# Kernel optimization log

Measured on AMD Instinct MI355X. Metric: run time of the kernel, lower is better.

## Reference

```python
import jax, jax.numpy as jnp
import numpy as np
import math

N_EMBD = 1024
N_HEAD = 16
HEAD_DIM = N_EMBD // N_HEAD
SCALE = 1.0 / math.sqrt(HEAD_DIM)


def setup_inputs() -> dict:
    key = jax.random.key(0)
    ks = jax.random.split(key, 5)
    B, S = 1, 4096
    std = 0.02
    x = jax.random.normal(ks[0], (B, S, N_EMBD), dtype=jnp.float32)
    # Linear weights stored as [in, out] (transposed vs torch storage; same math)
    w_qkv = jax.random.normal(ks[1], (N_EMBD, 3 * N_EMBD), dtype=jnp.float32) * std
    b_qkv = jnp.zeros((3 * N_EMBD,), dtype=jnp.float32)
    w_out = jax.random.normal(ks[2], (N_EMBD, N_EMBD), dtype=jnp.float32) * std
    b_out = jnp.zeros((N_EMBD,), dtype=jnp.float32)
    return {"x": x, "w_qkv": w_qkv, "b_qkv": b_qkv, "w_out": w_out, "b_out": b_out}


def reference(x, w_qkv, b_qkv, w_out, b_out):
    B, S, D = x.shape
    qkv = x @ w_qkv + b_qkv                      # [B, S, 3D]
    q, k, v = jnp.split(qkv, 3, axis=-1)
    # [B, H, S, d]
    q = q.reshape(B, S, N_HEAD, HEAD_DIM).transpose(0, 2, 1, 3)
    k = k.reshape(B, S, N_HEAD, HEAD_DIM).transpose(0, 2, 1, 3)
    v = v.reshape(B, S, N_HEAD, HEAD_DIM).transpose(0, 2, 1, 3)
    scores = jnp.einsum("bhqd,bhkd->bhqk", q, k) * SCALE  # [B, H, S, S]
    causal = jnp.tril(jnp.ones((S, S), dtype=bool))
    scores = jnp.where(causal, scores, -jnp.inf)
    attn = jax.nn.softmax(scores, axis=-1)
    out = jnp.einsum("bhqk,bhkd->bhqd", attn, v)  # [B, H, S, d]
    out = out.transpose(0, 2, 1, 3).reshape(B, S, D)
    return out @ w_out + b_out
```

## Files before the change

kernel.cpp:

```cpp
#include <hip/hip_runtime.h>
#include <hip/hip_bf16.h>
#include <cstdint>

typedef __bf16 bf16x8 __attribute__((ext_vector_type(8)));
typedef float  f32x4  __attribute__((ext_vector_type(4)));

#define S_LEN 4096
#define D_EMB 1024
#define N3    3072
#define HDIM  64

__device__ __forceinline__ unsigned short f2bf(float f) {
    union { unsigned int i; float f; } v; v.f = f;
    unsigned int i = v.i;
    return (unsigned short)((i + 0x7FFFu + ((i >> 16) & 1u)) >> 16);
}

__device__ __forceinline__ void async16(const void* g, void* l) {
    __builtin_amdgcn_global_load_lds(
        (const __attribute__((address_space(1))) unsigned int*)g,
        (__attribute__((address_space(3))) unsigned int*)l,
        16, 0, 0);
}

__global__ void convert_f32_bf16(const float* __restrict__ src,
                                 unsigned short* __restrict__ dst, int n8) {
    const int i = blockIdx.x * blockDim.x + threadIdx.x;
    if (i >= n8) return;
    float4 f0 = *(const float4*)&src[i * 8];
    float4 f1 = *(const float4*)&src[i * 8 + 4];
    union { uint4 q; unsigned short s[8]; } o;
    o.s[0]=f2bf(f0.x); o.s[1]=f2bf(f0.y); o.s[2]=f2bf(f0.z); o.s[3]=f2bf(f0.w);
    o.s[4]=f2bf(f1.x); o.s[5]=f2bf(f1.y); o.s[6]=f2bf(f1.z); o.s[7]=f2bf(f1.w);
    *(uint4*)&dst[i * 8] = o.q;
}

__global__ void transpose_f32_to_bf16(const float* __restrict__ src,
                                      unsigned short* __restrict__ dst,
                                      int R, int ld, int c0) {
    __shared__ float tile[32][33];
    const int tx = threadIdx.x, ty = threadIdx.y;
    const int r0 = blockIdx.y * 32, cc0 = blockIdx.x * 32;
    for (int i = 0; i < 32; i += 8)
        tile[ty + i][tx] = src[(size_t)(r0 + ty + i) * ld + c0 + cc0 + tx];
    __syncthreads();
    for (int i = 0; i < 32; i += 8)
        dst[(size_t)(cc0 + ty + i) * R + r0 + tx] = f2bf(tile[tx][ty + i]);
}

__global__ void transpose_bf16(const unsigned short* __restrict__ src,
                               unsigned short* __restrict__ dst,
                               int R, int ld, int c0) {
    __shared__ unsigned short tile[32][33];
    const int tx = threadIdx.x, ty = threadIdx.y;
    const int r0 = blockIdx.y * 32, cc0 = blockIdx.x * 32;
    for (int i = 0; i < 32; i += 8)
        tile[ty + i][tx] = src[(size_t)(r0 + ty + i) * ld + c0 + cc0 + tx];
    __syncthreads();
    for (int i = 0; i < 32; i += 8)
        dst[(size_t)(cc0 + ty + i) * R + r0 + tx] = tile[tx][ty + i];
}

template <bool OUT_F32>
__global__ __launch_bounds__(256) void gemm_bt_bias(
    const unsigned short* __restrict__ A,
    const unsigned short* __restrict__ BT,
    const float* __restrict__ bias,
    void* __restrict__ Cp,
    int M, int N, int K)
{
    __shared__ __align__(16) unsigned short As[128 * 32];
    __shared__ __align__(16) unsigned short Bs[128 * 32];
    const int tid  = threadIdx.x;
    const int wave = tid >> 6, lane = tid & 63;
    const int q4 = lane >> 4, l16 = lane & 15;
    const int m0 = blockIdx.y * 128, n0 = blockIdx.x * 128;
    const int wm = (wave >> 1) * 64, wn = (wave & 1) * 64;

    f32x4 acc[4][4] = {};

    const int srow = wave * 32 + (lane >> 2);
    const int scol = (lane & 3) * 8;

    for (int k0 = 0; k0 < K; k0 += 32) {
        __syncthreads();
        for (int i = 0; i < 2; ++i) {
            const int r = srow + i * 16;
            async16(A  + (size_t)(m0 + r) * K + k0 + scol,
                    &As[(wave * 32 + i * 16) * 32 + lane * 8]);
            async16(BT + (size_t)(n0 + r) * K + k0 + scol,
                    &Bs[(wave * 32 + i * 16) * 32 + lane * 8]);
        }
        __syncthreads();

        bf16x8 af[4], bfr[4];
        for (int mi = 0; mi < 4; ++mi)
            af[mi] = *(const bf16x8*)&As[(wm + mi * 16 + l16) * 32 + q4 * 8];
        for (int ni = 0; ni < 4; ++ni)
            bfr[ni] = *(const bf16x8*)&Bs[(wn + ni * 16 + l16) * 32 + q4 * 8];
        for (int mi = 0; mi < 4; ++mi)
            for (int ni = 0; ni < 4; ++ni)
                acc[mi][ni] = __builtin_amdgcn_mfma_f32_16x16x32_bf16(
                    af[mi], bfr[ni], acc[mi][ni], 0, 0, 0);
    }

    for (int ni = 0; ni < 4; ++ni) {
        const int col = n0 + wn + ni * 16 + l16;
        const float bv = bias[col];
        for (int mi = 0; mi < 4; ++mi) {
            const int row = m0 + wm + mi * 16 + q4 * 4;
            for (int r = 0; r < 4; ++r) {
                const float val = acc[mi][ni][r] + bv;
                if constexpr (OUT_F32)
                    ((float*)Cp)[(size_t)(row + r) * N + col] = val;
                else
                    ((unsigned short*)Cp)[(size_t)(row + r) * N + col] = f2bf(val);
            }
        }
    }
}

#define LDP 72
__global__ __launch_bounds__(256) void attn_flash(
    const unsigned short* __restrict__ qkv,
    const unsigned short* __restrict__ Vt,
    unsigned short* __restrict__ X2)
{
    __shared__ __align__(16) unsigned short Ks[64 * LDP];
    __shared__ __align__(16) unsigned short Vs[64 * LDP];
    __shared__ __align__(16) unsigned short Ps[4 * 16 * LDP];
    const int tid  = threadIdx.x;
    const int wave = tid >> 6, lane = tid & 63;
    const int q4 = lane >> 4, l16 = lane & 15;
    const int h  = blockIdx.y;

    const int x = blockIdx.x, hg = blockIdx.y >> 2;
    int qt;
    if      (hg == 0) qt = x;
    else if (hg == 1) qt = 63 - x;
    else if (hg == 2) qt = (x + 16) & 63;
    else              qt = (47 - x) & 63;
    const int q0 = qt * 64;

    bf16x8 aq[2];
    {
        const unsigned short* qp =
            qkv + (size_t)(q0 + wave * 16 + l16) * N3 + h * HDIM + q4 * 8;
        aq[0] = *(const bf16x8*)(qp);
        aq[1] = *(const bf16x8*)(qp + 32);
    }

    float l_part[4] = {0.f, 0.f, 0.f, 0.f};
    f32x4 o[4] = {};

    const int rr = tid >> 3;
    const int cc = (tid & 7) * 8;
    const int ntile = qt + 1;

    for (int t = 0; t < ntile; ++t) {
        const int kv0 = t * 64;
        uint4 kv_a = *(const uint4*)&qkv[(size_t)(kv0 + rr)      * N3 + D_EMB + h * HDIM + cc];
        uint4 kv_b = *(const uint4*)&qkv[(size_t)(kv0 + 32 + rr) * N3 + D_EMB + h * HDIM + cc];
        uint4 vt_a = *(const uint4*)&Vt [(size_t)(h * HDIM + rr)      * S_LEN + kv0 + cc];
        uint4 vt_b = *(const uint4*)&Vt [(size_t)(h * HDIM + 32 + rr) * S_LEN + kv0 + cc];
        __syncthreads();
        *(uint4*)&Ks[rr * LDP + cc]        = kv_a;
        *(uint4*)&Ks[(32 + rr) * LDP + cc] = kv_b;
        *(uint4*)&Vs[rr * LDP + cc]        = vt_a;
        *(uint4*)&Vs[(32 + rr) * LDP + cc] = vt_b;
        __syncthreads();

        f32x4 sacc[4] = {};
        for (int kk = 0; kk < 2; ++kk)
            for (int nt = 0; nt < 4; ++nt) {
                bf16x8 b = *(const bf16x8*)&Ks[(nt * 16 + l16) * LDP + kk * 32 + q4 * 8];
                sacc[nt] = __builtin_amdgcn_mfma_f32_16x16x32_bf16(
                    aq[kk], b, sacc[nt], 0, 0, 0);
            }

        const bool lastt = (t == ntile - 1);
        for (int r = 0; r < 4; ++r) {
            const int grow = q0 + wave * 16 + q4 * 4 + r;
            for (int nt = 0; nt < 4; ++nt) {
                float e = __expf(sacc[nt][r] * 0.125f);
                if (lastt && (kv0 + nt * 16 + l16 > grow)) e = 0.f;
                l_part[r] += e;
                Ps[wave * 16 * LDP + (q4 * 4 + r) * LDP + nt * 16 + l16] = f2bf(e);
            }
        }
        __asm__ volatile("s_waitcnt lgkmcnt(0)" ::: "memory");

        for (int kk = 0; kk < 2; ++kk) {
            bf16x8 pa = *(const bf16x8*)&Ps[wave * 16 * LDP + l16 * LDP + kk * 32 + q4 * 8];
            for (int dt = 0; dt < 4; ++dt) {
                bf16x8 vb = *(const bf16x8*)&Vs[(dt * 16 + l16) * LDP + kk * 32 + q4 * 8];
                o[dt] = __builtin_amdgcn_mfma_f32_16x16x32_bf16(pa, vb, o[dt], 0, 0, 0);
            }
        }
    }

    float linv[4];
    for (int r = 0; r < 4; ++r) {
        float l = l_part[r];
        for (int off = 1; off < 16; off <<= 1)
            l += __shfl_xor(l, off, 16);
        linv[r] = 1.f / l;
    }
    for (int dt = 0; dt < 4; ++dt)
        for (int r = 0; r < 4; ++r) {
            const int row = q0 + wave * 16 + q4 * 4 + r;
            X2[(size_t)row * D_EMB + h * HDIM + dt * 16 + l16] =
                f2bf(o[dt][r] * linv[r]);
        }
}

extern "C" void kernel_launch(void* const* d_in, const int* in_sizes, int n_in,
                              void* d_out, int out_size, void* d_ws, size_t ws_size,
                              hipStream_t stream) {
    const float* x     = (const float*)d_in[0];
    const float* w_qkv = (const float*)d_in[1];
    const float* b_qkv = (const float*)d_in[2];
    const float* w_out = (const float*)d_in[3];
    const float* b_out = (const float*)d_in[4];
    float* out = (float*)d_out;

    char* ws = (char*)d_ws;
    unsigned short* qkv   = (unsigned short*)(ws);
    unsigned short* wqkvT = (unsigned short*)(ws + 25165824);
    unsigned short* woutT = (unsigned short*)(ws + 31457280);
    unsigned short* Vt    = (unsigned short*)(ws + 33554432);
    unsigned short* X2    = (unsigned short*)(ws + 41943040);
    unsigned short* Xb    = X2;

    convert_f32_bf16<<<(4096 * 1024 / 8 + 255) / 256, 256, 0, stream>>>(
        x, Xb, 4096 * 1024 / 8);

    transpose_f32_to_bf16<<<dim3(3072 / 32, 1024 / 32), dim3(32, 8), 0, stream>>>(
        w_qkv, wqkvT, 1024, 3072, 0);
    transpose_f32_to_bf16<<<dim3(1024 / 32, 1024 / 32), dim3(32, 8), 0, stream>>>(
        w_out, woutT, 1024, 1024, 0);

    gemm_bt_bias<false><<<dim3(3072 / 128, 4096 / 128), 256, 0, stream>>>(
        Xb, wqkvT, b_qkv, qkv, 4096, 3072, 1024);

    transpose_bf16<<<dim3(1024 / 32, 4096 / 32), dim3(32, 8), 0, stream>>>(
        qkv, Vt, 4096, 3072, 2048);

    attn_flash<<<dim3(64, 16), 256, 0, stream>>>(qkv, Vt, X2);

    gemm_bt_bias<true><<<dim3(1024 / 128, 4096 / 128), 256, 0, stream>>>(
        X2, woutT, b_out, out, 4096, 1024, 1024);
}
```

Before: 247.2 us.

## Prefetch next KV tile into registers and transpose S MFMA for packed P stores

The K and V tile loads for step t+1 are issued into registers right after tile t is written to LDS, so global latency overlaps the QK^T and PV compute. The QK^T MFMA operands are swapped so each lane holds one query row across four key columns. This lets P be written to LDS as packed 64-bit stores instead of scalar 16-bit stores, and the row-sum reduction drops from 16 shuffles to a few. The cost is extra registers for the prefetched tile, which may lower occupancy.

After: 225.3 us. 1.1x faster.

```diff
diff --git a/kernel.cpp b/kernel.cpp
--- a/kernel.cpp
+++ b/kernel.cpp
@@ -150,43 +150,58 @@
         aq[1] = *(const bf16x8*)(qp + 32);
     }
 
-    float l_part[4] = {0.f, 0.f, 0.f, 0.f};
+    float l_part = 0.f;
     f32x4 o[4] = {};
 
     const int rr = tid >> 3;
     const int cc = (tid & 7) * 8;
     const int ntile = qt + 1;
+    const int grow = q0 + wave * 16 + l16;
+
+    uint4 kv_a, kv_b, vt_a, vt_b;
+    {
+        kv_a = *(const uint4*)&qkv[(size_t)(rr)      * N3 + D_EMB + h * HDIM + cc];
+        kv_b = *(const uint4*)&qkv[(size_t)(32 + rr) * N3 + D_EMB + h * HDIM + cc];
+        vt_a = *(const uint4*)&Vt [(size_t)(h * HDIM + rr)      * S_LEN + cc];
+        vt_b = *(const uint4*)&Vt [(size_t)(h * HDIM + 32 + rr) * S_LEN + cc];
+    }
 
     for (int t = 0; t < ntile; ++t) {
         const int kv0 = t * 64;
-        uint4 kv_a = *(const uint4*)&qkv[(size_t)(kv0 + rr)      * N3 + D_EMB + h * HDIM + cc];
-        uint4 kv_b = *(const uint4*)&qkv[(size_t)(kv0 + 32 + rr) * N3 + D_EMB + h * HDIM + cc];
-        uint4 vt_a = *(const uint4*)&Vt [(size_t)(h * HDIM + rr)      * S_LEN + kv0 + cc];
-        uint4 vt_b = *(const uint4*)&Vt [(size_t)(h * HDIM + 32 + rr) * S_LEN + kv0 + cc];
         __syncthreads();
         *(uint4*)&Ks[rr * LDP + cc]        = kv_a;
         *(uint4*)&Ks[(32 + rr) * LDP + cc] = kv_b;
         *(uint4*)&Vs[rr * LDP + cc]        = vt_a;
         *(uint4*)&Vs[(32 + rr) * LDP + cc] = vt_b;
+        if (t + 1 < ntile) {
+            const int kn = kv0 + 64;
+            kv_a = *(const uint4*)&qkv[(size_t)(kn + rr)      * N3 + D_EMB + h * HDIM + cc];
+            kv_b = *(const uint4*)&qkv[(size_t)(kn + 32 + rr) * N3 + D_EMB + h * HDIM + cc];
+            vt_a = *(const uint4*)&Vt [(size_t)(h * HDIM + rr)      * S_LEN + kn + cc];
+            vt_b = *(const uint4*)&Vt [(size_t)(h * HDIM + 32 + rr) * S_LEN + kn + cc];
+        }
         __syncthreads();
 
         f32x4 sacc[4] = {};
         for (int kk = 0; kk < 2; ++kk)
             for (int nt = 0; nt < 4; ++nt) {
-                bf16x8 b = *(const bf16x8*)&Ks[(nt * 16 + l16) * LDP + kk * 32 + q4 * 8];
+                bf16x8 kf = *(const bf16x8*)&Ks[(nt * 16 + l16) * LDP + kk * 32 + q4 * 8];
                 sacc[nt] = __builtin_amdgcn_mfma_f32_16x16x32_bf16(
-                    aq[kk], b, sacc[nt], 0, 0, 0);
+                    kf, aq[kk], sacc[nt], 0, 0, 0);
             }
 
         const bool lastt = (t == ntile - 1);
-        for (int r = 0; r < 4; ++r) {
-            const int grow = q0 + wave * 16 + q4 * 4 + r;
-            for (int nt = 0; nt < 4; ++nt) {
-                float e = __expf(sacc[nt][r] * 0.125f);
-                if (lastt && (kv0 + nt * 16 + l16 > grow)) e = 0.f;
-                l_part[r] += e;
-                Ps[wave * 16 * LDP + (q4 * 4 + r) * LDP + nt * 16 + l16] = f2bf(e);
-            }
+        for (int nt = 0; nt < 4; ++nt) {
+            float e[4];
+            for (int r = 0; r < 4; ++r) {
+                e[r] = __expf(sacc[nt][r] * 0.125f);
+                if (lastt && (kv0 + nt * 16 + q4 * 4 + r > grow)) e[r] = 0.f;
+                l_part += e[r];
+            }
+            union { uint2 q; unsigned short s[4]; } pk;
+            pk.s[0] = f2bf(e[0]); pk.s[1] = f2bf(e[1]);
+            pk.s[2] = f2bf(e[2]); pk.s[3] = f2bf(e[3]);
+            *(uint2*)&Ps[wave * 16 * LDP + l16 * LDP + nt * 16 + q4 * 4] = pk.q;
         }
         __asm__ volatile("s_waitcnt lgkmcnt(0)" ::: "memory");
 
@@ -199,13 +214,13 @@
         }
     }
 
+    float l = l_part;
+    l += __shfl_xor(l, 16);
+    l += __shfl_xor(l, 32);
     float linv[4];
-    for (int r = 0; r < 4; ++r) {
-        float l = l_part[r];
-        for (int off = 1; off < 16; off <<= 1)
-            l += __shfl_xor(l, off, 16);
-        linv[r] = 1.f / l;
-    }
+    for (int r = 0; r < 4; ++r)
+        linv[r] = 1.f / __shfl(l, q4 * 4 + r);
+
     for (int dt = 0; dt < 4; ++dt)
         for (int r = 0; r < 4; ++r) {
             const int row = q0 + wave * 16 + q4 * 4 + r;
```
